# Optimization experiments

Measured on AMD Instinct MI355X. Metric: run time of the kernel, lower is better.

Reference implementation:

```python
import jax, jax.numpy as jnp
import numpy as np

NEG_INF = -9e15
ALPHA = 0.2  # leaky relu slope


def setup_inputs() -> dict:
    key = jax.random.key(0)
    k1, k2, k3, k4 = jax.random.split(key, 4)
    B, N, Din = 8, 1024, 128
    H, D = 8, 16
    h = jax.random.normal(k1, (B, N, Din), dtype=jnp.float32)
    adj = jax.random.randint(k2, (B, N, N), 0, 2, dtype=jnp.int32)
    W = jax.random.normal(k3, (Din, H * D), dtype=jnp.float32) * 0.1
    a = jax.random.normal(k4, (H, 2 * D, 1), dtype=jnp.float32) * 0.1
    return {"h": h, "adj": adj, "W": W, "a": a}


def reference(h, adj, W, a):
    B, N, _ = h.shape
    H, twoD, _ = a.shape
    D = twoD // 2
    # Wh: [B, N, H, D]
    Wh = (h @ W).reshape(B, N, H, D)
    # Decompose additive attention: a . [Wh_i ; Wh_j] = a_src . Wh_i + a_dst . Wh_j
    a_src = a[:, :D, 0]   # [H, D]
    a_dst = a[:, D:, 0]   # [H, D]
    s_i = jnp.einsum('bnhd,hd->bhn', Wh, a_src)  # [B, H, N]
    s_j = jnp.einsum('bnhd,hd->bhn', Wh, a_dst)  # [B, H, N]
    scores = jax.nn.leaky_relu(s_i[:, :, :, None] + s_j[:, :, None, :], ALPHA)  # [B,H,N,N]
    scores = jnp.where(adj[:, None, :, :] == 0, NEG_INF, scores)
    attn = jax.nn.softmax(scores, axis=-1)  # [B, H, N, N]
    # Weighted aggregation over neighbors j
    h_prime = jnp.einsum('bhij,bjhd->bihd', attn, Wh).reshape(B, N, H * D)
    return h_prime
```

## Files before the change

### kernel.cpp

```cpp
#include <hip/hip_runtime.h>
#include <hip/hip_bf16.h>

constexpr int B   = 8;
constexpr int N   = 1024;
constexpr int DIN = 128;
constexpr int H   = 8;
constexpr int D   = 16;
constexpr int HD  = 128;
constexpr int TI  = 16;
constexpr int NS  = N / 32;

#define LOG2E 1.4426950408889634f
#define TCLAMP 30.0f

typedef __attribute__((ext_vector_type(8))) short bf16x8;
typedef __attribute__((ext_vector_type(4))) float f32x4;

__device__ inline float fast_exp2(float x) {
#if __has_builtin(__builtin_amdgcn_exp2f)
    return __builtin_amdgcn_exp2f(x);
#else
    return exp2f(x);
#endif
}

__global__ __launch_bounds__(256) void k_pack(const int* __restrict__ adj,
                                              unsigned int* __restrict__ bm)
{
    const size_t g = (size_t)blockIdx.x * 256 + threadIdx.x;
    const unsigned long long m = __ballot(adj[g] != 0);
    const int l = threadIdx.x & 63;
    if (l == 0)  bm[g >> 5] = (unsigned int)m;
    if (l == 32) bm[g >> 5] = (unsigned int)(m >> 32);
}

__global__ __launch_bounds__(256) void k_proj(
    const float* __restrict__ hsrc,
    const float* __restrict__ W,
    const float* __restrict__ a,
    __hip_bfloat16* __restrict__ WhT,
    float* __restrict__ tI,
    float* __restrict__ tJ)
{
    const int row0 = blockIdx.x * 32;
    const int b    = row0 >> 10;
    const int n0   = row0 & (N - 1);
    const int t    = threadIdx.x;
    const int lane = t & 63, wave = t >> 6;
    const int mn   = lane & 15, kg = lane >> 4;

    __shared__ __align__(16) __hip_bfloat16 hA[32][136];
    __shared__ __align__(16) __hip_bfloat16 Wt[128][136];

    {
        const float4* hf = reinterpret_cast<const float4*>(hsrc + (size_t)row0 * DIN);
        #pragma unroll
        for (int u = 0; u < 4; ++u) {
            const int idx = t + u * 256;
            const float4 v = hf[idx];
            const int r = idx >> 5, c4 = (idx & 31) * 4;
            hA[r][c4]     = __float2bfloat16(v.x);
            hA[r][c4 + 1] = __float2bfloat16(v.y);
            hA[r][c4 + 2] = __float2bfloat16(v.z);
            hA[r][c4 + 3] = __float2bfloat16(v.w);
        }
    }
    {
        const float4* wf = reinterpret_cast<const float4*>(W);
        #pragma unroll
        for (int u = 0; u < 16; ++u) {
            const int idx = t + u * 256;
            const float4 v = wf[idx];
            const int k = idx >> 5, c0 = (idx & 31) * 4;
            Wt[c0][k]     = __float2bfloat16(v.x);
            Wt[c0 + 1][k] = __float2bfloat16(v.y);
            Wt[c0 + 2][k] = __float2bfloat16(v.z);
            Wt[c0 + 3][k] = __float2bfloat16(v.w);
        }
    }
    __syncthreads();

    const int lr0 = (wave >> 1) * 16;
    const int ch  = wave & 1;
    f32x4 acc[4];
    #pragma unroll
    for (int f = 0; f < 4; ++f) acc[f] = (f32x4){0.f, 0.f, 0.f, 0.f};

    #pragma unroll
    for (int kk = 0; kk < 4; ++kk) {
        const bf16x8 af = *reinterpret_cast<const bf16x8*>(
            &hA[lr0 + mn][kk * 32 + kg * 8]);
        #pragma unroll
        for (int f = 0; f < 4; ++f) {
            const bf16x8 bf = *reinterpret_cast<const bf16x8*>(
                &Wt[ch * 64 + f * 16 + mn][kk * 32 + kg * 8]);
            acc[f] = __builtin_amdgcn_mfma_f32_16x16x32_bf16(af, bf, acc[f], 0, 0, 0);
        }
    }

    #pragma unroll
    for (int f = 0; f < 4; ++f) {
        const int hh = ch * 4 + f;
        const float as = a[hh * 32 + mn];
        const float ad = a[hh * 32 + 16 + mn];
        #pragma unroll
        for (int r = 0; r < 4; ++r) {
            const int n = n0 + lr0 + kg * 4 + r;
            WhT[((size_t)(b * HD + ch * 64 + f * 16 + mn)) * N + n] =
                __float2bfloat16(acc[f][r]);
            float vi = acc[f][r] * as;
            float vj = acc[f][r] * ad;
            #pragma unroll
            for (int m = 1; m < 16; m <<= 1) {
                vi += __shfl_xor(vi, m);
                vj += __shfl_xor(vj, m);
            }
            if (mn == 0) {
                tI[((size_t)(b * H + hh)) * N + n] = fminf(vi * LOG2E, TCLAMP);
                tJ[((size_t)(b * H + hh)) * N + n] = fminf(vj * LOG2E, TCLAMP);
            }
        }
    }
}

__global__ __launch_bounds__(256, 4) void k_attn(
    const unsigned int*   __restrict__ bm,
    const __hip_bfloat16* __restrict__ WhT,
    const float*          __restrict__ tI,
    const float*          __restrict__ tJ,
    float*                __restrict__ out)
{
    const int b    = blockIdx.y;
    const int i0   = blockIdx.x * TI;
    const int lane = threadIdx.x & 63;
    const int h    = blockIdx.z * 4 + (threadIdx.x >> 6);
    const int mn   = lane & 15, kg = lane >> 4;

    const float Arow = tI[((size_t)(b * H + h)) * N + i0 + mn];
    const float* tjrow = tJ + ((size_t)(b * H + h)) * N + kg * 8;
    const __hip_bfloat16* wrow =
        WhT + ((size_t)(b * HD + h * 16 + mn)) * N + kg * 8;
    const unsigned int* brow = bm + ((size_t)(b * N) + i0 + mn) * (N / 32);

    unsigned int mw[NS];
    {
        const uint4* bq = reinterpret_cast<const uint4*>(brow);
        #pragma unroll
        for (int u = 0; u < 8; ++u) {
            const uint4 v = bq[u];
            mw[4 * u + 0] = v.x; mw[4 * u + 1] = v.y;
            mw[4 * u + 2] = v.z; mw[4 * u + 3] = v.w;
        }
    }

    f32x4 accO = {0.f, 0.f, 0.f, 0.f};
    f32x4 accD = {0.f, 0.f, 0.f, 0.f};
    bf16x8 ones;
    #pragma unroll
    for (int e = 0; e < 8; ++e) ones[e] = (short)0x3F80;

    float4 t0c = *reinterpret_cast<const float4*>(tjrow);
    float4 t1c = *reinterpret_cast<const float4*>(tjrow + 4);
    bf16x8 wc  = *reinterpret_cast<const bf16x8*>(wrow);

    #pragma unroll
    for (int s = 0; s < NS; ++s) {
        float4 t0n, t1n; bf16x8 wn;
        if (s < NS - 1) {
            const int off = (s + 1) * 32;
            t0n = *reinterpret_cast<const float4*>(tjrow + off);
            t1n = *reinterpret_cast<const float4*>(tjrow + off + 4);
            wn  = *reinterpret_cast<const bf16x8*>(wrow + off);
            asm volatile("" ::: "memory");
        }

        const unsigned int m8 = (mw[s] >> (kg * 8)) & 0xFFu;
        const float tv[8] = {t0c.x, t0c.y, t0c.z, t0c.w,
                             t1c.x, t1c.y, t1c.z, t1c.w};
        bf16x8 af;
        #pragma unroll
        for (int e = 0; e < 8; ++e) {
            const float x = Arow + tv[e];
            float sc = fmaxf(x, 0.2f * x);
            sc = ((m8 >> e) & 1u) ? sc : -1.0e30f;
            af[e] = (short)__bfloat16_as_ushort(
                __float2bfloat16(fast_exp2(sc)));
        }
        accO = __builtin_amdgcn_mfma_f32_16x16x32_bf16(af, wc, accO, 0, 0, 0);
        accD = __builtin_amdgcn_mfma_f32_16x16x32_bf16(af, ones, accD, 0, 0, 0);

        if (s < NS - 1) { t0c = t0n; t1c = t1n; wc = wn; }
    }

    #pragma unroll
    for (int r = 0; r < 4; ++r) {
        out[((size_t)(b * N) + i0 + kg * 4 + r) * HD + h * 16 + mn] =
            accO[r] / accD[r];
    }
}

extern "C" void kernel_launch(void* const* d_in, const int* in_sizes, int n_in,
                              void* d_out, int out_size, void* d_ws, size_t ws_size,
                              hipStream_t stream)
{
    const float* h   = (const float*)d_in[0];
    const int*   adj = (const int*)d_in[1];
    const float* W   = (const float*)d_in[2];
    const float* a   = (const float*)d_in[3];
    float* out = (float*)d_out;

    float* ws = (float*)d_ws;
    float* tI = ws;
    float* tJ = ws + (size_t)B * H * N;
    __hip_bfloat16* WhT = (__hip_bfloat16*)(ws + (size_t)2 * B * H * N);
    unsigned int* bm = (unsigned int*)((char*)WhT +
                       (size_t)B * N * HD * sizeof(__hip_bfloat16));

    k_pack<<<dim3((B * N * N) / 256), dim3(256), 0, stream>>>(adj, bm);
    k_proj<<<dim3(B * N / 32), dim3(256), 0, stream>>>(h, W, a, WhT, tI, tJ);
    k_attn<<<dim3(N / TI, B, 2), dim3(256), 0, stream>>>(bm, WhT, tI, tJ, out);
}
```

Before: 54.70 us.

## Fuse adjacency packing into projection kernel and reorder bitmask bytes for attention

```diff
diff --git a/kernel.cpp b/kernel.cpp
--- a/kernel.cpp
+++ b/kernel.cpp
@@ -8,7 +8,6 @@
 constexpr int D   = 16;
 constexpr int HD  = 128;
 constexpr int TI  = 16;
-constexpr int NS  = N / 32;
 
 #define LOG2E 1.4426950408889634f
 #define TCLAMP 30.0f
@@ -24,33 +23,41 @@
 #endif
 }
 
-__global__ __launch_bounds__(256) void k_pack(const int* __restrict__ adj,
-                                              unsigned int* __restrict__ bm)
-{
-    const size_t g = (size_t)blockIdx.x * 256 + threadIdx.x;
-    const unsigned long long m = __ballot(adj[g] != 0);
-    const int l = threadIdx.x & 63;
-    if (l == 0)  bm[g >> 5] = (unsigned int)m;
-    if (l == 32) bm[g >> 5] = (unsigned int)(m >> 32);
-}
-
-__global__ __launch_bounds__(256) void k_proj(
+__global__ __launch_bounds__(256) void k_prep(
     const float* __restrict__ hsrc,
     const float* __restrict__ W,
     const float* __restrict__ a,
+    const int*   __restrict__ adj,
+    unsigned char* __restrict__ bmR,
     __hip_bfloat16* __restrict__ WhT,
     float* __restrict__ tI,
     float* __restrict__ tJ)
 {
+    __shared__ __align__(16) __hip_bfloat16 hA[32][136];
+    __shared__ __align__(16) __hip_bfloat16 Wt[128][136];
+
+    if (blockIdx.x >= 256) {
+        const size_t g = (size_t)(blockIdx.x - 256) * 256 + threadIdx.x;
+        const unsigned long long m = __ballot(adj[g] != 0);
+        if ((threadIdx.x & 63) == 0) {
+            const size_t row = g >> 10;
+            const int s0 = (int)(g & 1023) >> 5;
+            unsigned char* dst = bmR + row * 128;
+            #pragma unroll
+            for (int kg = 0; kg < 4; ++kg) {
+                dst[kg * 32 + s0]     = (unsigned char)((m >> (kg * 8)) & 0xFFull);
+                dst[kg * 32 + s0 + 1] = (unsigned char)((m >> (32 + kg * 8)) & 0xFFull);
+            }
+        }
+        return;
+    }
+
     const int row0 = blockIdx.x * 32;
     const int b    = row0 >> 10;
     const int n0   = row0 & (N - 1);
     const int t    = threadIdx.x;
     const int lane = t & 63, wave = t >> 6;
     const int mn   = lane & 15, kg = lane >> 4;
-
-    __shared__ __align__(16) __hip_bfloat16 hA[32][136];
-    __shared__ __align__(16) __hip_bfloat16 Wt[128][136];
 
     {
         const float4* hf = reinterpret_cast<const float4*>(hsrc + (size_t)row0 * DIN);
@@ -124,7 +131,7 @@
 }
 
 __global__ __launch_bounds__(256, 4) void k_attn(
-    const unsigned int*   __restrict__ bm,
+    const unsigned char*  __restrict__ bmR,
     const __hip_bfloat16* __restrict__ WhT,
     const float*          __restrict__ tI,
     const float*          __restrict__ tJ,
@@ -135,23 +142,14 @@
     const int lane = threadIdx.x & 63;
     const int h    = blockIdx.z * 4 + (threadIdx.x >> 6);
     const int mn   = lane & 15, kg = lane >> 4;
-
-    const float Arow = tI[((size_t)(b * H + h)) * N + i0 + mn];
+    const int row  = i0 + mn;
+
+    const float Arow = tI[((size_t)(b * H + h)) * N + row];
     const float* tjrow = tJ + ((size_t)(b * H + h)) * N + kg * 8;
     const __hip_bfloat16* wrow =
         WhT + ((size_t)(b * HD + h * 16 + mn)) * N + kg * 8;
-    const unsigned int* brow = bm + ((size_t)(b * N) + i0 + mn) * (N / 32);
-
-    unsigned int mw[NS];
-    {
-        const uint4* bq = reinterpret_cast<const uint4*>(brow);
-        #pragma unroll
-        for (int u = 0; u < 8; ++u) {
-            const uint4 v = bq[u];
-            mw[4 * u + 0] = v.x; mw[4 * u + 1] = v.y;
-            mw[4 * u + 2] = v.z; mw[4 * u + 3] = v.w;
-        }
-    }
+    const unsigned char* mrow =
+        bmR + ((size_t)(b * N) + row) * 128 + kg * 32;
 
     f32x4 accO = {0.f, 0.f, 0.f, 0.f};
     f32x4 accD = {0.f, 0.f, 0.f, 0.f};
@@ -159,37 +157,36 @@
     #pragma unroll
     for (int e = 0; e < 8; ++e) ones[e] = (short)0x3F80;
 
-    float4 t0c = *reinterpret_cast<const float4*>(tjrow);
-    float4 t1c = *reinterpret_cast<const float4*>(tjrow + 4);
-    bf16x8 wc  = *reinterpret_cast<const bf16x8*>(wrow);
-
-    #pragma unroll
-    for (int s = 0; s < NS; ++s) {
-        float4 t0n, t1n; bf16x8 wn;
-        if (s < NS - 1) {
-            const int off = (s + 1) * 32;
-            t0n = *reinterpret_cast<const float4*>(tjrow + off);
-            t1n = *reinterpret_cast<const float4*>(tjrow + off + 4);
-            wn  = *reinterpret_cast<const bf16x8*>(wrow + off);
-            asm volatile("" ::: "memory");
-        }
-
-        const unsigned int m8 = (mw[s] >> (kg * 8)) & 0xFFu;
-        const float tv[8] = {t0c.x, t0c.y, t0c.z, t0c.w,
-                             t1c.x, t1c.y, t1c.z, t1c.w};
-        bf16x8 af;
-        #pragma unroll
-        for (int e = 0; e < 8; ++e) {
-            const float x = Arow + tv[e];
-            float sc = fmaxf(x, 0.2f * x);
-            sc = ((m8 >> e) & 1u) ? sc : -1.0e30f;
-            af[e] = (short)__bfloat16_as_ushort(
-                __float2bfloat16(fast_exp2(sc)));
-        }
-        accO = __builtin_amdgcn_mfma_f32_16x16x32_bf16(af, wc, accO, 0, 0, 0);
-        accD = __builtin_amdgcn_mfma_f32_16x16x32_bf16(af, ones, accD, 0, 0, 0);
-
-        if (s < NS - 1) { t0c = t0n; t1c = t1n; wc = wn; }
+    for (int sq = 0; sq < 8; ++sq) {
+        const int j0 = sq * 128;
+
+        const unsigned int mv =
+            *reinterpret_cast<const unsigned int*>(mrow + sq * 4);
+        float4 ta[4], tb[4]; bf16x8 wv[4];
+        #pragma unroll
+        for (int q = 0; q < 4; ++q) {
+            ta[q] = *reinterpret_cast<const float4*>(tjrow + j0 + q * 32);
+            tb[q] = *reinterpret_cast<const float4*>(tjrow + j0 + q * 32 + 4);
+            wv[q] = *reinterpret_cast<const bf16x8*>(wrow + j0 + q * 32);
+        }
+
+        #pragma unroll
+        for (int q = 0; q < 4; ++q) {
+            const unsigned int m8 = (mv >> (q * 8)) & 0xFFu;
+            const float tv[8] = {ta[q].x, ta[q].y, ta[q].z, ta[q].w,
+                                 tb[q].x, tb[q].y, tb[q].z, tb[q].w};
+            bf16x8 af;
+            #pragma unroll
+            for (int e = 0; e < 8; ++e) {
+                const float x = Arow + tv[e];
+                float sc = fmaxf(x, 0.2f * x);
+                sc = ((m8 >> e) & 1u) ? sc : -1.0e30f;
+                af[e] = (short)__bfloat16_as_ushort(
+                    __float2bfloat16(fast_exp2(sc)));
+            }
+            accO = __builtin_amdgcn_mfma_f32_16x16x32_bf16(af, wv[q], accO, 0, 0, 0);
+            accD = __builtin_amdgcn_mfma_f32_16x16x32_bf16(af, ones, accD, 0, 0, 0);
+        }
     }
 
     #pragma unroll
@@ -213,10 +210,10 @@
     float* tI = ws;
     float* tJ = ws + (size_t)B * H * N;
     __hip_bfloat16* WhT = (__hip_bfloat16*)(ws + (size_t)2 * B * H * N);
-    unsigned int* bm = (unsigned int*)((char*)WhT +
-                       (size_t)B * N * HD * sizeof(__hip_bfloat16));
-
-    k_pack<<<dim3((B * N * N) / 256), dim3(256), 0, stream>>>(adj, bm);
-    k_proj<<<dim3(B * N / 32), dim3(256), 0, stream>>>(h, W, a, WhT, tI, tJ);
-    k_attn<<<dim3(N / TI, B, 2), dim3(256), 0, stream>>>(bm, WhT, tI, tJ, out);
-}
+    unsigned char* bmR = (unsigned char*)((char*)WhT +
+                         (size_t)B * N * HD * sizeof(__hip_bfloat16));
+
+    k_prep<<<dim3(256 + (B * N * N) / 256), dim3(256), 0, stream>>>(
+        h, W, a, adj, bmR, WhT, tI, tJ);
+    k_attn<<<dim3(N / TI, B, 2), dim3(256), 0, stream>>>(bmR, WhT, tI, tJ, out);
+}
```

New measurement: 64.47 us. 17.9% more time.
